# Kernel tuning notes

Measured on AMD Instinct MI355X. Metric: run time of the kernel, lower is better.

## Reference

```python
import jax, jax.numpy as jnp
import numpy as np

BS, PV, NPTS, C = 8, 40000, 32, 4   # batch, pillars/sample (=max_voxels), max_num_points, point channels
X_L, Y_L = 432, 496                  # BEV grid from voxel_size / point_cloud_range


def setup_inputs() -> dict:
    key = jax.random.key(0)
    k1, k2, k3 = jax.random.split(key, 3)
    # (P, num_points, c) voxelized point features
    pillars = jax.random.normal(k1, (BS * PV, NPTS, C), dtype=jnp.float32)
    # unique BEV cell per pillar within each sample (voxelizer never emits duplicate coords)
    perms = jax.vmap(lambda k: jax.random.permutation(k, X_L * Y_L)[:PV])(
        jax.random.split(k2, BS))  # (BS, PV) linear cell ids
    xs = (perms // Y_L).reshape(-1)
    ys = (perms % Y_L).reshape(-1)
    b = jnp.repeat(jnp.arange(BS, dtype=jnp.int32), PV)
    z = jnp.zeros_like(b)
    coors_batch = jnp.stack([b, xs.astype(jnp.int32), ys.astype(jnp.int32), z], axis=1)  # (P, 4)
    npoints_per_pillar = jax.random.randint(k3, (BS * PV,), 1, NPTS + 1, dtype=jnp.int32)
    return {
        "pillars": pillars,
        "coors_batch": coors_batch,
        "npoints_per_pillar": npoints_per_pillar,
        "bs": BS, "x_l": X_L, "y_l": Y_L,
    }


def reference(pillars, coors_batch, npoints_per_pillar, bs, x_l, y_l):
    # per-pillar xyz center of mass: sum over (zero-padded) points / true point count
    center_pt = jnp.sum(pillars[:, :, :3], axis=1) / npoints_per_pillar[:, None].astype(jnp.float32)  # (P, 3)
    # scatter centers into dense BEV canvas (bs, x_l, y_l, 3); coords unique -> set semantics match torch assignment
    canvas = jnp.zeros((bs, x_l, y_l, 3), dtype=jnp.float32)
    canvas = canvas.at[coors_batch[:, 0], coors_batch[:, 1], coors_batch[:, 2]].set(center_pt)
    # per-sample permute(2,1,0): (x_l,y_l,3) -> (3,y_l,x_l)
    batched_pillar_center = jnp.transpose(canvas, (0, 3, 2, 1))
    return (pillars, coors_batch, npoints_per_pillar, batched_pillar_center)
```

## Files before the change

kernel.cpp:

```cpp
#include <hip/hip_runtime.h>


typedef float vfloat4 __attribute__((ext_vector_type(4)));

__global__ __launch_bounds__(256) void canvas_zero(float4* __restrict__ dst, long n4) {
    long i = (long)blockIdx.x * blockDim.x + threadIdx.x;
    const long stride = (long)gridDim.x * blockDim.x;
    const float4 z = make_float4(0.f, 0.f, 0.f, 0.f);
    for (; i < n4; i += stride) dst[i] = z;
}

__global__ __launch_bounds__(256) void pillar_fused(
    const vfloat4* __restrict__ pillars4,
    const int4* __restrict__ coors4,
    const int* __restrict__ npoints,
    const int* __restrict__ xlp,
    const int* __restrict__ ylp,
    vfloat4* __restrict__ out_pillars4,
    float4* __restrict__ out_coors4,
    float* __restrict__ out_np,
    float* __restrict__ canvas,
    int P)
{
    const int tid  = threadIdx.x;
    const int g    = tid >> 4;
    const int r    = tid & 15;
    const int p    = blockIdx.x * 16 + g;
    if (p >= P) return;

    const long b0 = (long)p * 32;

    const vfloat4 v0 = __builtin_nontemporal_load(&pillars4[b0 + r]);
    const vfloat4 v1 = __builtin_nontemporal_load(&pillars4[b0 + r + 16]);
    out_pillars4[b0 + r]      = v0;
    out_pillars4[b0 + r + 16] = v1;

    float sx = v0.x + v1.x, sy = v0.y + v1.y, sz = v0.z + v1.z;
    #pragma unroll
    for (int m = 8; m >= 1; m >>= 1) {
        sx += __shfl_xor(sx, m);
        sy += __shfl_xor(sy, m);
        sz += __shfl_xor(sz, m);
    }

    if (r < 3) {
        const int4 c   = coors4[p];
        const int npts = npoints[p];
        const float s  = (r == 0) ? sx : (r == 1) ? sy : sz;
        const float val = s / (float)npts;

        const int x_l = *xlp;
        const int y_l = *ylp;
        const long cs   = (long)y_l * (long)x_l;
        const long base = (long)c.x * 3l * cs + (long)c.z * (long)x_l + (long)c.y;
        canvas[base + (long)r * cs] = val;

        if (r == 0) {
            out_coors4[p] = make_float4((float)c.x, (float)c.y, (float)c.z, (float)c.w);
            out_np[p]     = (float)npts;
        }
    }
}

extern "C" void kernel_launch(void* const* d_in, const int* in_sizes, int n_in,
                              void* d_out, int out_size, void* d_ws, size_t ws_size,
                              hipStream_t stream) {
    const vfloat4* pillars4 = (const vfloat4*)d_in[0];
    const int4* coors4      = (const int4*)d_in[1];
    const int* npoints      = (const int*)d_in[2];
    const int* xlp = (const int*)d_in[4];
    const int* ylp = (const int*)d_in[5];

    const int n_pillars = in_sizes[0];
    const int n_coors   = in_sizes[1];
    const int P         = in_sizes[2];

    float* out            = (float*)d_out;
    vfloat4* out_pillars4 = (vfloat4*)out;
    float* out_coors      = out + n_pillars;
    float* out_np         = out_coors + n_coors;
    float* canvas         = out_np + P;
    const long canvas_elems = (long)out_size - n_pillars - n_coors - P;

    const long n4 = canvas_elems >> 2;
    int zblocks = (int)((n4 + 511) / 512);
    if (zblocks > 2048) zblocks = 2048;
    canvas_zero<<<zblocks, 256, 0, stream>>>((float4*)canvas, n4);

    const int blocks = (P + 15) / 16;
    pillar_fused<<<blocks, 256, 0, stream>>>(
        pillars4, coors4, npoints, xlp, ylp,
        out_pillars4, (float4*)out_coors, out_np, canvas, P);
}
```

Before: 72.25 us.

## Fuse canvas zeroing and pillar scatter into one cooperative kernel with grid sync

Replaces the separate zero-fill kernel and pillar kernel with one cooperative kernel that zeroes the canvas, does a grid-wide barrier, then processes pillars in a grid-stride loop over a fixed 1024-block grid. The aim is to remove one kernel launch and the gap between the two kernels. The cost is a grid-wide sync, cooperative-launch overhead, and a smaller persistent grid that may hide memory latency less well during the pillar copy phase.

```diff
diff --git a/kernel.cpp b/kernel.cpp
--- a/kernel.cpp
+++ b/kernel.cpp
@@ -1,16 +1,10 @@
 #include <hip/hip_runtime.h>
+#include <hip/hip_cooperative_groups.h>
 
 
 typedef float vfloat4 __attribute__((ext_vector_type(4)));
 
-__global__ __launch_bounds__(256) void canvas_zero(float4* __restrict__ dst, long n4) {
-    long i = (long)blockIdx.x * blockDim.x + threadIdx.x;
-    const long stride = (long)gridDim.x * blockDim.x;
-    const float4 z = make_float4(0.f, 0.f, 0.f, 0.f);
-    for (; i < n4; i += stride) dst[i] = z;
-}
-
-__global__ __launch_bounds__(256) void pillar_fused(
+__global__ __launch_bounds__(256) void pillar_coop(
     const vfloat4* __restrict__ pillars4,
     const int4* __restrict__ coors4,
     const int* __restrict__ npoints,
@@ -19,45 +13,59 @@
     vfloat4* __restrict__ out_pillars4,
     float4* __restrict__ out_coors4,
     float* __restrict__ out_np,
-    float* __restrict__ canvas,
+    float4* __restrict__ canvas4,
+    long n4,
     int P)
 {
-    const int tid  = threadIdx.x;
-    const int g    = tid >> 4;
-    const int r    = tid & 15;
-    const int p    = blockIdx.x * 16 + g;
-    if (p >= P) return;
+    {
+        const long stride = (long)gridDim.x * blockDim.x;
+        const float4 z = make_float4(0.f, 0.f, 0.f, 0.f);
+        for (long i = (long)blockIdx.x * blockDim.x + threadIdx.x; i < n4; i += stride)
+            canvas4[i] = z;
+    }
+    cooperative_groups::this_grid().sync();
 
-    const long b0 = (long)p * 32;
+    float* __restrict__ canvas = (float*)canvas4;
+    const int tid = threadIdx.x;
+    const int g   = tid >> 4;
+    const int r   = tid & 15;
+    const int x_l = *xlp;
+    const int y_l = *ylp;
+    const long cs = (long)y_l * (long)x_l;
+    const int nchunks = (P + 15) >> 4;
 
-    const vfloat4 v0 = __builtin_nontemporal_load(&pillars4[b0 + r]);
-    const vfloat4 v1 = __builtin_nontemporal_load(&pillars4[b0 + r + 16]);
-    out_pillars4[b0 + r]      = v0;
-    out_pillars4[b0 + r + 16] = v1;
+    for (int chunk = blockIdx.x; chunk < nchunks; chunk += gridDim.x) {
+        const int p = chunk * 16 + g;
+        if (p >= P) continue;
 
-    float sx = v0.x + v1.x, sy = v0.y + v1.y, sz = v0.z + v1.z;
-    #pragma unroll
-    for (int m = 8; m >= 1; m >>= 1) {
-        sx += __shfl_xor(sx, m);
-        sy += __shfl_xor(sy, m);
-        sz += __shfl_xor(sz, m);
-    }
+        const long b0 = (long)p * 32;
 
-    if (r < 3) {
-        const int4 c   = coors4[p];
-        const int npts = npoints[p];
-        const float s  = (r == 0) ? sx : (r == 1) ? sy : sz;
-        const float val = s / (float)npts;
+        const vfloat4 v0 = __builtin_nontemporal_load(&pillars4[b0 + r]);
+        const vfloat4 v1 = __builtin_nontemporal_load(&pillars4[b0 + r + 16]);
+        out_pillars4[b0 + r]      = v0;
+        out_pillars4[b0 + r + 16] = v1;
 
-        const int x_l = *xlp;
-        const int y_l = *ylp;
-        const long cs   = (long)y_l * (long)x_l;
-        const long base = (long)c.x * 3l * cs + (long)c.z * (long)x_l + (long)c.y;
-        canvas[base + (long)r * cs] = val;
+        float sx = v0.x + v1.x, sy = v0.y + v1.y, sz = v0.z + v1.z;
+        #pragma unroll
+        for (int m = 8; m >= 1; m >>= 1) {
+            sx += __shfl_xor(sx, m);
+            sy += __shfl_xor(sy, m);
+            sz += __shfl_xor(sz, m);
+        }
 
-        if (r == 0) {
-            out_coors4[p] = make_float4((float)c.x, (float)c.y, (float)c.z, (float)c.w);
-            out_np[p]     = (float)npts;
+        if (r < 3) {
+            const int4 c   = coors4[p];
+            const int npts = npoints[p];
+            const float s  = (r == 0) ? sx : (r == 1) ? sy : sz;
+            const float val = s / (float)npts;
+
+            const long base = (long)c.x * 3l * cs + (long)c.z * (long)x_l + (long)c.y;
+            canvas[base + (long)r * cs] = val;
+
+            if (r == 0) {
+                out_coors4[p] = make_float4((float)c.x, (float)c.y, (float)c.z, (float)c.w);
+                out_np[p]     = (float)npts;
+            }
         }
     }
 }
@@ -80,15 +88,15 @@
     float* out_coors      = out + n_pillars;
     float* out_np         = out_coors + n_coors;
     float* canvas         = out_np + P;
-    const long canvas_elems = (long)out_size - n_pillars - n_coors - P;
+    long canvas_elems     = (long)out_size - n_pillars - n_coors - P;
+    long n4               = canvas_elems >> 2;
 
-    const long n4 = canvas_elems >> 2;
-    int zblocks = (int)((n4 + 511) / 512);
-    if (zblocks > 2048) zblocks = 2048;
-    canvas_zero<<<zblocks, 256, 0, stream>>>((float4*)canvas, n4);
-
-    const int blocks = (P + 15) / 16;
-    pillar_fused<<<blocks, 256, 0, stream>>>(
-        pillars4, coors4, npoints, xlp, ylp,
-        out_pillars4, (float4*)out_coors, out_np, canvas, P);
+    dim3 grid(1024), block(256);
+    void* args[] = {
+        (void*)&pillars4, (void*)&coors4, (void*)&npoints,
+        (void*)&xlp, (void*)&ylp,
+        (void*)&out_pillars4, (void*)&out_coors, (void*)&out_np,
+        (void*)&canvas, (void*)&n4, (void*)&P
+    };
+    hipLaunchCooperativeKernel((const void*)pillar_coop, grid, block, args, 0, stream);
 }
```

After: 161.7 us. 2.24x slower.
